# Kernel tuning notes

Hardware: AMD Instinct MI355X
Metric: run time of the kernel (lower is better)

The kernel has to match this reference:

```python
import jax, jax.numpy as jnp
import numpy as np

N_NODES = 50000
N_EDGES = 1600000
IN_DIM = 128
HIDDEN = 16
HEADS = 8
OUT_DIM = 64


def setup_inputs() -> dict:
    key = jax.random.key(0)
    k1, k2, k3, k4, k5 = jax.random.split(key, 5)
    h = jax.random.normal(k1, (N_NODES, IN_DIM), dtype=jnp.float32)
    W1 = jax.random.normal(k2, (IN_DIM, HEADS * HIDDEN), dtype=jnp.float32) * (IN_DIM ** -0.5)
    W2 = jax.random.normal(k3, (HEADS * HIDDEN, OUT_DIM), dtype=jnp.float32) * ((HEADS * HIDDEN) ** -0.5)
    src = jax.random.randint(k4, (N_EDGES,), 0, N_NODES, dtype=jnp.int32)
    dst = jax.random.randint(k5, (N_EDGES,), 0, N_NODES, dtype=jnp.int32)
    return {"h": h, "W1": W1, "W2": W2, "src": src, "dst": dst}


def dot_gat_conv(h, W, src, dst, num_heads, out_feats):
    # Project and split heads: [N, H, D]
    feat = (h @ W).reshape(-1, num_heads, out_feats)
    fs = feat[src]                       # [E, H, D] gather
    fd = feat[dst]                       # [E, H, D] gather
    scale = jnp.asarray(out_feats, feat.dtype) ** -0.5
    e = jnp.einsum('ehd,ehd->eh', fs, fd) * scale  # [E, H] scaled dot score
    # Edge softmax over incoming edges of each destination node
    m = jax.ops.segment_max(e, dst, num_segments=N_NODES)   # [N, H]
    m = jnp.where(jnp.isfinite(m), m, jnp.zeros_like(m))    # isolated nodes
    ex = jnp.exp(e - m[dst])                                 # [E, H]
    denom = jax.ops.segment_sum(ex, dst, num_segments=N_NODES)  # [N, H]
    a = ex / jnp.maximum(denom[dst], jnp.asarray(1e-9, ex.dtype))  # [E, H]
    # Weighted scatter-sum aggregation: [N, H, D]
    return jax.ops.segment_sum(a[:, :, None] * fs, dst, num_segments=N_NODES)


def reference(h, W1, W2, src, dst):
    h1 = dot_gat_conv(h, W1, src, dst, HEADS, HIDDEN)  # [N, H, hidden]
    h1 = jax.nn.elu(h1).reshape(N_NODES, HEADS * HIDDEN)  # flatten(1)
    # Dropout: eval-mode identity
    h2 = dot_gat_conv(h1, W2, src, dst, 1, OUT_DIM)  # [N, 1, out]
    return h2.mean(axis=1)  # [N, out]
```

## Files before the change

### kernel.cpp

```cpp
#include <hip/hip_runtime.h>
#include <hip/hip_bf16.h>

#define N_NODES 50000
#define N_EDGES 1600000
#define NBUCK 98
#define EPB 4096
#define NB_A ((N_EDGES + EPB - 1) / EPB)

typedef short bf16x8 __attribute__((ext_vector_type(8)));
typedef float f32x4  __attribute__((ext_vector_type(4)));
typedef float f32x2  __attribute__((ext_vector_type(2)));

__device__ __forceinline__ float bf16_raw_to_f32(unsigned short u) {
    return __uint_as_float(((unsigned)u) << 16);
}
__device__ __forceinline__ unsigned short f32_to_bf16_raw(float v) {
    unsigned u = __float_as_uint(v);
    return (unsigned short)((u + 0x7fffu + ((u >> 16) & 1u)) >> 16);
}
__device__ __forceinline__ float load_elem(const void* p, size_t i, int f) {
    if (f) return ((const float*)p)[i];
    return bf16_raw_to_f32(((const unsigned short*)p)[i]);
}
__device__ __forceinline__ void unpack8v(uint4 u, f32x2* f) {
    f[0] = (f32x2){__uint_as_float(u.x << 16), __uint_as_float(u.x & 0xffff0000u)};
    f[1] = (f32x2){__uint_as_float(u.y << 16), __uint_as_float(u.y & 0xffff0000u)};
    f[2] = (f32x2){__uint_as_float(u.z << 16), __uint_as_float(u.z & 0xffff0000u)};
    f[3] = (f32x2){__uint_as_float(u.w << 16), __uint_as_float(u.w & 0xffff0000u)};
}

__global__ void detect_dtype_kernel(const unsigned short* __restrict__ w1raw,
                                    int* __restrict__ flag, int* __restrict__ bcnt) {
    __shared__ float red[256];
    if (threadIdx.x < NBUCK) bcnt[threadIdx.x] = 0;
    float mx = 0.f;
    for (int i = threadIdx.x * 2; i < 16384; i += 512) {
        float v = fabsf(bf16_raw_to_f32(w1raw[i]));
        if (!isnan(v)) mx = fmaxf(mx, v);
    }
    red[threadIdx.x] = mx;
    __syncthreads();
    for (int s = 128; s > 0; s >>= 1) {
        if (threadIdx.x < s) red[threadIdx.x] = fmaxf(red[threadIdx.x], red[threadIdx.x + s]);
        __syncthreads();
    }
    if (threadIdx.x == 0) flag[0] = (red[0] > 1e4f) ? 1 : 0;
}

#define WPAD 136
__global__ void prep_kernel(const void* __restrict__ W1, const void* __restrict__ W2,
                            unsigned short* __restrict__ W1T,
                            unsigned short* __restrict__ W2T,
                            const int* __restrict__ flag) {
    const int f = *flag;
    int bid = blockIdx.x, tid = threadIdx.x;
    if (bid < 8) {
        int n = bid * 16 + (tid & 15);
        int kb = (tid >> 4) * 8;
        for (int j = 0; j < 8; ++j)
            W1T[n * WPAD + kb + j] = f32_to_bf16_raw(load_elem(W1, (size_t)(kb + j) * 128 + n, f));
    } else {
        int n = (bid - 8) * 16 + (tid & 15);
        int kb = (tid >> 4) * 8;
        for (int j = 0; j < 8; ++j)
            W2T[n * WPAD + kb + j] = f32_to_bf16_raw(load_elem(W2, (size_t)(kb + j) * 64 + n, f));
    }
}

__global__ void bucket_count_kernel(const int* __restrict__ dst,
                                    int* __restrict__ bcnt, int E) {
    __shared__ int hist[NBUCK];
    int t = threadIdx.x;
    if (t < NBUCK) hist[t] = 0;
    __syncthreads();
    int e0 = blockIdx.x * EPB;
    for (int k = 0; k < 16; ++k) {
        int e = e0 + k * 256 + t;
        if (e < E) atomicAdd(&hist[dst[e] >> 9], 1);
    }
    __syncthreads();
    if (t < NBUCK && hist[t]) atomicAdd(&bcnt[t], hist[t]);
}

__global__ void bucket_scan_kernel(const int* __restrict__ bcnt,
                                   int* __restrict__ bbase, int* __restrict__ bcur) {
    __shared__ int tmp[128];
    int t = threadIdx.x;
    int v = (t < NBUCK) ? bcnt[t] : 0;
    tmp[t] = v;
    __syncthreads();
    for (int off = 1; off < 128; off <<= 1) {
        int x = (t >= off) ? tmp[t - off] : 0;
        __syncthreads();
        tmp[t] += x;
        __syncthreads();
    }
    if (t < NBUCK) { int ex = tmp[t] - v; bbase[t] = ex; bcur[t] = ex; }
    if (t == NBUCK - 1) bbase[NBUCK] = tmp[t];
}

__global__ void binA_kernel(const int* __restrict__ src, const int* __restrict__ dst,
                            int* __restrict__ bcur, unsigned* __restrict__ inter, int E) {
    __shared__ int hist[NBUCK], gbase[NBUCK], cur[NBUCK];
    int t = threadIdx.x;
    if (t < NBUCK) hist[t] = 0;
    __syncthreads();
    int e0 = blockIdx.x * EPB;
    for (int k = 0; k < 16; ++k) {
        int e = e0 + k * 256 + t;
        if (e < E) atomicAdd(&hist[dst[e] >> 9], 1);
    }
    __syncthreads();
    if (t < NBUCK) {
        int hv = hist[t];
        gbase[t] = hv ? atomicAdd(&bcur[t], hv) : 0;
        cur[t] = 0;
    }
    __syncthreads();
    for (int k = 0; k < 16; ++k) {
        int e = e0 + k * 256 + t;
        if (e < E) {
            int d = dst[e];
            int b = d >> 9;
            int off = atomicAdd(&cur[b], 1);
            inter[gbase[b] + off] = (unsigned)src[e] | ((unsigned)(d & 511) << 16);
        }
    }
}

__global__ void binB_kernel(const unsigned* __restrict__ inter,
                            const int* __restrict__ bbase,
                            int* __restrict__ csr_src, int* __restrict__ start,
                            int N, int E) {
    int b = blockIdx.x;
    int node0 = b << 9;
    int lo = bbase[b], hi = bbase[b + 1];
    __shared__ int hist[512];
    __shared__ int t2[256];
    int t = threadIdx.x;
    hist[t] = 0; hist[t + 256] = 0;
    __syncthreads();
    for (int e = lo + t; e < hi; e += 256) atomicAdd(&hist[inter[e] >> 16], 1);
    __syncthreads();
    int s0 = hist[2 * t], s1 = hist[2 * t + 1];
    t2[t] = s0 + s1;
    __syncthreads();
    for (int off = 1; off < 256; off <<= 1) {
        int x = (t >= off) ? t2[t - off] : 0;
        __syncthreads();
        t2[t] += x;
        __syncthreads();
    }
    int base = (t == 0) ? 0 : t2[t - 1];
    hist[2 * t] = base;
    hist[2 * t + 1] = base + s0;
    __syncthreads();
    int nodeCnt = min(512, N - node0);
    for (int i = t; i < nodeCnt; i += 256) start[node0 + i] = lo + hist[i];
    if (b == NBUCK - 1 && t == 0) start[N] = E;
    __syncthreads();
    for (int e = lo + t; e < hi; e += 256) {
        unsigned u = inter[e];
        int slot = lo + atomicAdd(&hist[u >> 16], 1);
        csr_src[slot] = (int)(u & 0xffffu);
    }
}

__global__ void gemm1_mfma_kernel(const void* __restrict__ h,
                                  const unsigned short* __restrict__ W1T,
                                  unsigned short* __restrict__ feat1, int N,
                                  const int* __restrict__ flag) {
    const int f = *flag;
    int lane = threadIdx.x & 63;
    int rbase = blockIdx.x * 64 + (threadIdx.x >> 6) * 16;
    int arow = rbase + (lane & 15);
    int arowc = min(arow, N - 1);
    int kb0 = (lane >> 4) * 8;

    f32x4 acc[8];
#pragma unroll
    for (int t = 0; t < 8; ++t) acc[t] = (f32x4){0.f, 0.f, 0.f, 0.f};

#pragma unroll
    for (int ks = 0; ks < 4; ++ks) {
        int kb = ks * 32 + kb0;
        bf16x8 afrag;
        if (f == 0) {
            afrag = *(const bf16x8*)((const unsigned short*)h + (size_t)arowc * 128 + kb);
        } else {
            const float* hp = (const float*)h + (size_t)arowc * 128 + kb;
#pragma unroll
            for (int j = 0; j < 8; ++j) afrag[j] = (short)f32_to_bf16_raw(hp[j]);
        }
#pragma unroll
        for (int t = 0; t < 8; ++t) {
            int n = t * 16 + (lane & 15);
            bf16x8 bfrag = *(const bf16x8*)(W1T + n * WPAD + kb);
            acc[t] = __builtin_amdgcn_mfma_f32_16x16x32_bf16(afrag, bfrag, acc[t], 0, 0, 0);
        }
    }
    int orow0 = rbase + (lane >> 4) * 4;
    int col = lane & 15;
#pragma unroll
    for (int t = 0; t < 8; ++t)
#pragma unroll
        for (int r = 0; r < 4; ++r) {
            int row = orow0 + r;
            if (row < N)
                feat1[(size_t)row * 128 + t * 16 + col] = f32_to_bf16_raw(acc[t][r]);
        }
}

__global__ void gemm2_mfma_kernel(const unsigned short* __restrict__ agg1e,
                                  const unsigned short* __restrict__ W2T,
                                  unsigned short* __restrict__ feat2, int N) {
    int lane = threadIdx.x & 63;
    int rbase = blockIdx.x * 64 + (threadIdx.x >> 6) * 16;
    int arow = rbase + (lane & 15);
    int arowc = min(arow, N - 1);
    int kb0 = (lane >> 4) * 8;

    f32x4 acc[4];
#pragma unroll
    for (int t = 0; t < 4; ++t) acc[t] = (f32x4){0.f, 0.f, 0.f, 0.f};

#pragma unroll
    for (int ks = 0; ks < 4; ++ks) {
        int kb = ks * 32 + kb0;
        bf16x8 afrag = *(const bf16x8*)(agg1e + (size_t)arowc * 128 + kb);
#pragma unroll
        for (int t = 0; t < 4; ++t) {
            int n = t * 16 + (lane & 15);
            bf16x8 bfrag = *(const bf16x8*)(W2T + n * WPAD + kb);
            acc[t] = __builtin_amdgcn_mfma_f32_16x16x32_bf16(afrag, bfrag, acc[t], 0, 0, 0);
        }
    }
    int orow0 = rbase + (lane >> 4) * 4;
    int col = lane & 15;
#pragma unroll
    for (int t = 0; t < 4; ++t)
#pragma unroll
        for (int r = 0; r < 4; ++r) {
            int row = orow0 + r;
            if (row < N)
                feat2[(size_t)row * 64 + t * 16 + col] = f32_to_bf16_raw(acc[t][r]);
        }
}

__global__ void gat1_kernel(const unsigned short* __restrict__ feat1,
                            const int* __restrict__ csr_src,
                            const int* __restrict__ start,
                            unsigned short* __restrict__ agg1e, int N) {
    int wave = blockIdx.x * 4 + (threadIdx.x >> 6);
    if (wave >= N) return;
    int lane = threadIdx.x & 63;
    int grp = lane >> 4, gl = lane & 15;
    const char* fb = (const char*)feat1;
    unsigned loff = (unsigned)gl << 4;
    f32x2 fd2[4];
    unpack8v(*(const uint4*)(fb + (((unsigned)wave << 8) + loff)), fd2);

    float l = 0.f;
    f32x2 acc2[4];
#pragma unroll
    for (int k = 0; k < 4; ++k) acc2[k] = (f32x2){0.f, 0.f};

    int e0 = start[wave], e1 = start[wave + 1];
    int base = e0;
    for (; base + 8 <= e1; base += 8) {
        int s0 = csr_src[base + grp];
        int s1 = csr_src[base + 4 + grp];
        uint4 u0 = *(const uint4*)(fb + (((unsigned)s0 << 8) + loff));
        uint4 u1 = *(const uint4*)(fb + (((unsigned)s1 << 8) + loff));
        f32x2 f02[4], f12[4];
        unpack8v(u0, f02); unpack8v(u1, f12);
        f32x2 p02 = fd2[0] * f02[0];
        f32x2 p12 = fd2[0] * f12[0];
#pragma unroll
        for (int k = 1; k < 4; ++k) { p02 += fd2[k] * f02[k]; p12 += fd2[k] * f12[k]; }
        float p0 = p02.x + p02.y;
        float p1 = p12.x + p12.y;
        p0 += __shfl_xor(p0, 1);
        p1 += __shfl_xor(p1, 1);
        float w0 = __expf(p0 * 0.25f);
        float w1 = __expf(p1 * 0.25f);
        f32x2 w02 = (f32x2){w0, w0}, w12 = (f32x2){w1, w1};
#pragma unroll
        for (int k = 0; k < 4; ++k) {
            acc2[k] += w02 * f02[k];
            acc2[k] += w12 * f12[k];
        }
        l += w0 + w1;
    }
    for (; base < e1; base += 4) {
        int ed = base + grp;
        bool act = ed < e1;
        int s = act ? csr_src[ed] : 0;
        uint4 u = *(const uint4*)(fb + (((unsigned)s << 8) + loff));
        f32x2 fv2[4]; unpack8v(u, fv2);
        f32x2 p2 = fd2[0] * fv2[0];
#pragma unroll
        for (int k = 1; k < 4; ++k) p2 += fd2[k] * fv2[k];
        float p = p2.x + p2.y;
        p += __shfl_xor(p, 1);
        float w = act ? __expf(p * 0.25f) : 0.f;
        f32x2 wv = (f32x2){w, w};
#pragma unroll
        for (int k = 0; k < 4; ++k) acc2[k] += wv * fv2[k];
        l += w;
    }
#pragma unroll
    for (int off = 16; off <= 32; off <<= 1) {
        l += __shfl_xor(l, off);
#pragma unroll
        for (int k = 0; k < 4; ++k) {
            acc2[k].x += __shfl_xor(acc2[k].x, off);
            acc2[k].y += __shfl_xor(acc2[k].y, off);
        }
    }
    if (grp == 0) {
        float rcp = 1.f / fmaxf(l, 1e-9f);
        float v[8];
#pragma unroll
        for (int k = 0; k < 4; ++k) {
            float x0 = acc2[k].x * rcp;
            float x1 = acc2[k].y * rcp;
            v[2 * k]     = (x0 > 0.f) ? x0 : expm1f(x0);
            v[2 * k + 1] = (x1 > 0.f) ? x1 : expm1f(x1);
        }
        uint4 pk;
        pk.x = (unsigned)f32_to_bf16_raw(v[0]) | ((unsigned)f32_to_bf16_raw(v[1]) << 16);
        pk.y = (unsigned)f32_to_bf16_raw(v[2]) | ((unsigned)f32_to_bf16_raw(v[3]) << 16);
        pk.z = (unsigned)f32_to_bf16_raw(v[4]) | ((unsigned)f32_to_bf16_raw(v[5]) << 16);
        pk.w = (unsigned)f32_to_bf16_raw(v[6]) | ((unsigned)f32_to_bf16_raw(v[7]) << 16);
        *(uint4*)(agg1e + (size_t)wave * 128 + gl * 8) = pk;
    }
}

__global__ void gat2_kernel(const unsigned short* __restrict__ feat2,
                            const int* __restrict__ csr_src,
                            const int* __restrict__ start,
                            void* __restrict__ out, int N,
                            const int* __restrict__ flag) {
    int wave = blockIdx.x * 4 + (threadIdx.x >> 6);
    if (wave >= N) return;
    int lane = threadIdx.x & 63;
    int grp = lane >> 3, gl = lane & 7;
    const int f = *flag;
    const char* fb = (const char*)feat2;
    unsigned loff = (unsigned)gl << 4;
    f32x2 fd2[4];
    unpack8v(*(const uint4*)(fb + (((unsigned)wave << 7) + loff)), fd2);

    float l = 0.f;
    f32x2 acc2[4];
#pragma unroll
    for (int k = 0; k < 4; ++k) acc2[k] = (f32x2){0.f, 0.f};

    int e0 = start[wave], e1 = start[wave + 1];
    int base = e0;
    for (; base + 16 <= e1; base += 16) {
        int s0 = csr_src[base + grp];
        int s1 = csr_src[base + 8 + grp];
        uint4 u0 = *(const uint4*)(fb + (((unsigned)s0 << 7) + loff));
        uint4 u1 = *(const uint4*)(fb + (((unsigned)s1 << 7) + loff));
        f32x2 f02[4], f12[4];
        unpack8v(u0, f02); unpack8v(u1, f12);
        f32x2 p02 = fd2[0] * f02[0];
        f32x2 p12 = fd2[0] * f12[0];
#pragma unroll
        for (int k = 1; k < 4; ++k) { p02 += fd2[k] * f02[k]; p12 += fd2[k] * f12[k]; }
        float p0 = p02.x + p02.y;
        float p1 = p12.x + p12.y;
        p0 += __shfl_xor(p0, 1); p1 += __shfl_xor(p1, 1);
        p0 += __shfl_xor(p0, 2); p1 += __shfl_xor(p1, 2);
        p0 += __shfl_xor(p0, 4); p1 += __shfl_xor(p1, 4);
        float w0 = __expf(p0 * 0.125f);
        float w1 = __expf(p1 * 0.125f);
        f32x2 w02 = (f32x2){w0, w0}, w12 = (f32x2){w1, w1};
#pragma unroll
        for (int k = 0; k < 4; ++k) {
            acc2[k] += w02 * f02[k];
            acc2[k] += w12 * f12[k];
        }
        l += w0 + w1;
    }
    for (; base < e1; base += 8) {
        int ed = base + grp;
        bool act = ed < e1;
        int s = act ? csr_src[ed] : 0;
        uint4 u = *(const uint4*)(fb + (((unsigned)s << 7) + loff));
        f32x2 fv2[4]; unpack8v(u, fv2);
        f32x2 p2 = fd2[0] * fv2[0];
#pragma unroll
        for (int k = 1; k < 4; ++k) p2 += fd2[k] * fv2[k];
        float p = p2.x + p2.y;
        p += __shfl_xor(p, 1);
        p += __shfl_xor(p, 2);
        p += __shfl_xor(p, 4);
        float w = act ? __expf(p * 0.125f) : 0.f;
        f32x2 wv = (f32x2){w, w};
#pragma unroll
        for (int k = 0; k < 4; ++k) acc2[k] += wv * fv2[k];
        l += w;
    }
#pragma unroll
    for (int off = 8; off <= 32; off <<= 1) {
        l += __shfl_xor(l, off);
#pragma unroll
        for (int k = 0; k < 4; ++k) {
            acc2[k].x += __shfl_xor(acc2[k].x, off);
            acc2[k].y += __shfl_xor(acc2[k].y, off);
        }
    }
    if (grp == 0) {
        float rcp = 1.f / fmaxf(l, 1e-9f);
        float v[8];
#pragma unroll
        for (int k = 0; k < 4; ++k) {
            v[2 * k]     = acc2[k].x * rcp;
            v[2 * k + 1] = acc2[k].y * rcp;
        }
        if (f) {
            float* op = (float*)out + (size_t)wave * 64 + gl * 8;
            *(float4*)(op)     = (float4){v[0], v[1], v[2], v[3]};
            *(float4*)(op + 4) = (float4){v[4], v[5], v[6], v[7]};
        } else {
            uint4 pk;
            pk.x = (unsigned)f32_to_bf16_raw(v[0]) | ((unsigned)f32_to_bf16_raw(v[1]) << 16);
            pk.y = (unsigned)f32_to_bf16_raw(v[2]) | ((unsigned)f32_to_bf16_raw(v[3]) << 16);
            pk.z = (unsigned)f32_to_bf16_raw(v[4]) | ((unsigned)f32_to_bf16_raw(v[5]) << 16);
            pk.w = (unsigned)f32_to_bf16_raw(v[6]) | ((unsigned)f32_to_bf16_raw(v[7]) << 16);
            *(uint4*)((unsigned short*)out + (size_t)wave * 64 + gl * 8) = pk;
        }
    }
}

extern "C" void kernel_launch(void* const* d_in, const int* in_sizes, int n_in,
                              void* d_out, int out_size, void* d_ws, size_t ws_size,
                              hipStream_t stream) {
    const void* h  = d_in[0];
    const void* W1 = d_in[1];
    const void* W2 = d_in[2];
    const int* src = (const int*)d_in[3];
    const int* dst = (const int*)d_in[4];

    float* ws = (float*)d_ws;
    unsigned short* feat1 = (unsigned short*)ws;
    unsigned short* agg1e = (unsigned short*)(ws + 3200000);
    unsigned short* feat2 = (unsigned short*)ws;
    unsigned* inter       = (unsigned*)(ws + 6400000);
    int*   csr_src        = (int*)(ws + 9600000);
    int*   start          = (int*)(ws + 11200000);
    int*   flag           = (int*)(ws + 11330000);
    int*   bcnt           = (int*)(ws + 11331000);
    int*   bbase          = (int*)(ws + 11332000);
    int*   bcur           = (int*)(ws + 11333000);
    unsigned short* W1T   = (unsigned short*)(ws + 11340000);
    unsigned short* W2T   = (unsigned short*)(ws + 11350000);

    detect_dtype_kernel<<<1, 256, 0, stream>>>((const unsigned short*)W1, flag, bcnt);
    prep_kernel<<<12, 256, 0, stream>>>(W1, W2, W1T, W2T, flag);

    bucket_count_kernel<<<NB_A, 256, 0, stream>>>(dst, bcnt, N_EDGES);
    bucket_scan_kernel<<<1, 128, 0, stream>>>(bcnt, bbase, bcur);
    binA_kernel<<<NB_A, 256, 0, stream>>>(src, dst, bcur, inter, N_EDGES);
    binB_kernel<<<NBUCK, 256, 0, stream>>>(inter, bbase, csr_src, start, N_NODES, N_EDGES);

    gemm1_mfma_kernel<<<(N_NODES + 63) / 64, 256, 0, stream>>>(h, W1T, feat1, N_NODES, flag);
    gat1_kernel<<<(N_NODES + 3) / 4, 256, 0, stream>>>(feat1, csr_src, start, agg1e, N_NODES);
    gemm2_mfma_kernel<<<(N_NODES + 63) / 64, 256, 0, stream>>>(agg1e, W2T, feat2, N_NODES);
    gat2_kernel<<<(N_NODES + 3) / 4, 256, 0, stream>>>(feat2, csr_src, start, d_out, N_NODES, flag);
}
```

Baseline: 283.5 us.

## Sort nodes by degree and process eight destination nodes per wave

Adds a degree histogram in binB, a scan, and a scatter that builds a worklist of nodes sorted by in-degree, highest first. The gat kernels now assign 8 destination nodes per wave, 8 lanes per node, so lanes in a wave have similar edge counts. Each lane covers 16 features in gat1 and 8 in gat2, which removes most cross-group shuffle reductions and the masked tail iterations. The cost is two extra small launches, atomics on the degree counters, and output writes to scattered node rows. Each node's edge list is now walked serially by its 8 lanes, two edges at a time.

```diff
diff --git a/kernel.cpp b/kernel.cpp
--- a/kernel.cpp
+++ b/kernel.cpp
@@ -6,6 +6,7 @@
 #define NBUCK 98
 #define EPB 4096
 #define NB_A ((N_EDGES + EPB - 1) / EPB)
+#define DEGBINS 512
 
 typedef short bf16x8 __attribute__((ext_vector_type(8)));
 typedef float f32x4  __attribute__((ext_vector_type(4)));
@@ -30,9 +31,12 @@
 }
 
 __global__ void detect_dtype_kernel(const unsigned short* __restrict__ w1raw,
-                                    int* __restrict__ flag, int* __restrict__ bcnt) {
+                                    int* __restrict__ flag, int* __restrict__ bcnt,
+                                    int* __restrict__ ghist) {
     __shared__ float red[256];
     if (threadIdx.x < NBUCK) bcnt[threadIdx.x] = 0;
+    ghist[threadIdx.x] = 0;
+    ghist[threadIdx.x + 256] = 0;
     float mx = 0.f;
     for (int i = threadIdx.x * 2; i < 16384; i += 512) {
         float v = fabsf(bf16_raw_to_f32(w1raw[i]));
@@ -131,6 +135,7 @@
 __global__ void binB_kernel(const unsigned* __restrict__ inter,
                             const int* __restrict__ bbase,
                             int* __restrict__ csr_src, int* __restrict__ start,
+                            int* __restrict__ ghist,
                             int N, int E) {
     int b = blockIdx.x;
     int node0 = b << 9;
@@ -143,6 +148,9 @@
     for (int e = lo + t; e < hi; e += 256) atomicAdd(&hist[inter[e] >> 16], 1);
     __syncthreads();
     int s0 = hist[2 * t], s1 = hist[2 * t + 1];
+    int nodeCnt = min(512, N - node0);
+    if (2 * t < nodeCnt)     atomicAdd(&ghist[min(s0, DEGBINS - 1)], 1);
+    if (2 * t + 1 < nodeCnt) atomicAdd(&ghist[min(s1, DEGBINS - 1)], 1);
     t2[t] = s0 + s1;
     __syncthreads();
     for (int off = 1; off < 256; off <<= 1) {
@@ -155,7 +163,6 @@
     hist[2 * t] = base;
     hist[2 * t + 1] = base + s0;
     __syncthreads();
-    int nodeCnt = min(512, N - node0);
     for (int i = t; i < nodeCnt; i += 256) start[node0 + i] = lo + hist[i];
     if (b == NBUCK - 1 && t == 0) start[N] = E;
     __syncthreads();
@@ -164,6 +171,31 @@
         int slot = lo + atomicAdd(&hist[u >> 16], 1);
         csr_src[slot] = (int)(u & 0xffffu);
     }
+}
+
+__global__ void degscan_kernel(const int* __restrict__ ghist, int* __restrict__ gcur) {
+    __shared__ int tmp[DEGBINS];
+    int t = threadIdx.x;
+    int v = ghist[t];
+    tmp[t] = v;
+    __syncthreads();
+    for (int off = 1; off < DEGBINS; off <<= 1) {
+        int x = (t >= off) ? tmp[t - off] : 0;
+        __syncthreads();
+        tmp[t] += x;
+        __syncthreads();
+    }
+    gcur[t] = tmp[t] - v;
+}
+
+__global__ void degscatter_kernel(const int* __restrict__ start,
+                                  int* __restrict__ gcur,
+                                  int* __restrict__ wl, int N) {
+    int i = blockIdx.x * 256 + threadIdx.x;
+    if (i >= N) return;
+    int deg = start[i + 1] - start[i];
+    int off = atomicAdd(&gcur[min(deg, DEGBINS - 1)], 1);
+    wl[N - 1 - off] = i;
 }
 
 __global__ void gemm1_mfma_kernel(const void* __restrict__ h,
@@ -250,189 +282,170 @@
 __global__ void gat1_kernel(const unsigned short* __restrict__ feat1,
                             const int* __restrict__ csr_src,
                             const int* __restrict__ start,
+                            const int* __restrict__ wl,
                             unsigned short* __restrict__ agg1e, int N) {
     int wave = blockIdx.x * 4 + (threadIdx.x >> 6);
-    if (wave >= N) return;
     int lane = threadIdx.x & 63;
-    int grp = lane >> 4, gl = lane & 15;
+    int g = lane >> 3, gl = lane & 7;
+    int nidx = wave * 8 + g;
+    if (nidx >= N) return;
+    int dstn = wl[nidx];
+
     const char* fb = (const char*)feat1;
+    unsigned loff = (unsigned)gl << 5;
+    unsigned drow = ((unsigned)dstn << 8) + loff;
+    f32x2 fd2[8];
+    unpack8v(*(const uint4*)(fb + drow), fd2);
+    unpack8v(*(const uint4*)(fb + drow + 16), fd2 + 4);
+
+    float l = 0.f;
+    f32x2 acc2[8];
+#pragma unroll
+    for (int k = 0; k < 8; ++k) acc2[k] = (f32x2){0.f, 0.f};
+
+    int e0 = start[dstn], e1 = start[dstn + 1];
+    int base = e0;
+    for (; base + 2 <= e1; base += 2) {
+        int s0 = csr_src[base], s1 = csr_src[base + 1];
+        const char* r0 = fb + ((unsigned)s0 << 8) + loff;
+        const char* r1 = fb + ((unsigned)s1 << 8) + loff;
+        uint4 a0 = *(const uint4*)r0, a1 = *(const uint4*)(r0 + 16);
+        uint4 b0 = *(const uint4*)r1, b1 = *(const uint4*)(r1 + 16);
+        f32x2 f0[8], f1[8];
+        unpack8v(a0, f0); unpack8v(a1, f0 + 4);
+        unpack8v(b0, f1); unpack8v(b1, f1 + 4);
+        f32x2 p0 = fd2[0] * f0[0];
+        f32x2 p1 = fd2[0] * f1[0];
+#pragma unroll
+        for (int k = 1; k < 8; ++k) { p0 += fd2[k] * f0[k]; p1 += fd2[k] * f1[k]; }
+        float q0 = p0.x + p0.y;
+        float q1 = p1.x + p1.y;
+        float w0 = __expf(q0 * 0.25f);
+        float w1 = __expf(q1 * 0.25f);
+        f32x2 W0 = (f32x2){w0, w0}, W1 = (f32x2){w1, w1};
+#pragma unroll
+        for (int k = 0; k < 8; ++k) {
+            acc2[k] += W0 * f0[k];
+            acc2[k] += W1 * f1[k];
+        }
+        l += w0 + w1;
+    }
+    if (base < e1) {
+        int s = csr_src[base];
+        const char* r0 = fb + ((unsigned)s << 8) + loff;
+        uint4 a0 = *(const uint4*)r0, a1 = *(const uint4*)(r0 + 16);
+        f32x2 fv[8];
+        unpack8v(a0, fv); unpack8v(a1, fv + 4);
+        f32x2 p = fd2[0] * fv[0];
+#pragma unroll
+        for (int k = 1; k < 8; ++k) p += fd2[k] * fv[k];
+        float w = __expf((p.x + p.y) * 0.25f);
+        f32x2 W = (f32x2){w, w};
+#pragma unroll
+        for (int k = 0; k < 8; ++k) acc2[k] += W * fv[k];
+        l += w;
+    }
+    float rcp = 1.f / fmaxf(l, 1e-9f);
+    unsigned pk[8];
+#pragma unroll
+    for (int k = 0; k < 8; ++k) {
+        float x0 = acc2[k].x * rcp, x1 = acc2[k].y * rcp;
+        x0 = (x0 > 0.f) ? x0 : expm1f(x0);
+        x1 = (x1 > 0.f) ? x1 : expm1f(x1);
+        pk[k] = (unsigned)f32_to_bf16_raw(x0) | ((unsigned)f32_to_bf16_raw(x1) << 16);
+    }
+    *(uint4*)((char*)agg1e + drow)      = (uint4){pk[0], pk[1], pk[2], pk[3]};
+    *(uint4*)((char*)agg1e + drow + 16) = (uint4){pk[4], pk[5], pk[6], pk[7]};
+}
+
+__global__ void gat2_kernel(const unsigned short* __restrict__ feat2,
+                            const int* __restrict__ csr_src,
+                            const int* __restrict__ start,
+                            const int* __restrict__ wl,
+                            void* __restrict__ out, int N,
+                            const int* __restrict__ flag) {
+    int wave = blockIdx.x * 4 + (threadIdx.x >> 6);
+    int lane = threadIdx.x & 63;
+    int g = lane >> 3, gl = lane & 7;
+    int nidx = wave * 8 + g;
+    if (nidx >= N) return;
+    int dstn = wl[nidx];
+    const int f = *flag;
+
+    const char* fb = (const char*)feat2;
     unsigned loff = (unsigned)gl << 4;
+    unsigned drow = ((unsigned)dstn << 7) + loff;
     f32x2 fd2[4];
-    unpack8v(*(const uint4*)(fb + (((unsigned)wave << 8) + loff)), fd2);
+    unpack8v(*(const uint4*)(fb + drow), fd2);
 
     float l = 0.f;
     f32x2 acc2[4];
 #pragma unroll
     for (int k = 0; k < 4; ++k) acc2[k] = (f32x2){0.f, 0.f};
 
-    int e0 = start[wave], e1 = start[wave + 1];
+    int e0 = start[dstn], e1 = start[dstn + 1];
     int base = e0;
-    for (; base + 8 <= e1; base += 8) {
-        int s0 = csr_src[base + grp];
-        int s1 = csr_src[base + 4 + grp];
-        uint4 u0 = *(const uint4*)(fb + (((unsigned)s0 << 8) + loff));
-        uint4 u1 = *(const uint4*)(fb + (((unsigned)s1 << 8) + loff));
-        f32x2 f02[4], f12[4];
-        unpack8v(u0, f02); unpack8v(u1, f12);
-        f32x2 p02 = fd2[0] * f02[0];
-        f32x2 p12 = fd2[0] * f12[0];
-#pragma unroll
-        for (int k = 1; k < 4; ++k) { p02 += fd2[k] * f02[k]; p12 += fd2[k] * f12[k]; }
-        float p0 = p02.x + p02.y;
-        float p1 = p12.x + p12.y;
-        p0 += __shfl_xor(p0, 1);
-        p1 += __shfl_xor(p1, 1);
-        float w0 = __expf(p0 * 0.25f);
-        float w1 = __expf(p1 * 0.25f);
-        f32x2 w02 = (f32x2){w0, w0}, w12 = (f32x2){w1, w1};
+    for (; base + 2 <= e1; base += 2) {
+        int s0 = csr_src[base], s1 = csr_src[base + 1];
+        uint4 u0 = *(const uint4*)(fb + ((unsigned)s0 << 7) + loff);
+        uint4 u1 = *(const uint4*)(fb + ((unsigned)s1 << 7) + loff);
+        f32x2 f0[4], f1[4];
+        unpack8v(u0, f0); unpack8v(u1, f1);
+        f32x2 p0 = fd2[0] * f0[0];
+        f32x2 p1 = fd2[0] * f1[0];
+#pragma unroll
+        for (int k = 1; k < 4; ++k) { p0 += fd2[k] * f0[k]; p1 += fd2[k] * f1[k]; }
+        float q0 = p0.x + p0.y;
+        float q1 = p1.x + p1.y;
+        q0 += __shfl_xor(q0, 1); q1 += __shfl_xor(q1, 1);
+        q0 += __shfl_xor(q0, 2); q1 += __shfl_xor(q1, 2);
+        q0 += __shfl_xor(q0, 4); q1 += __shfl_xor(q1, 4);
+        float w0 = __expf(q0 * 0.125f);
+        float w1 = __expf(q1 * 0.125f);
+        f32x2 W0 = (f32x2){w0, w0}, W1 = (f32x2){w1, w1};
 #pragma unroll
         for (int k = 0; k < 4; ++k) {
-            acc2[k] += w02 * f02[k];
-            acc2[k] += w12 * f12[k];
+            acc2[k] += W0 * f0[k];
+            acc2[k] += W1 * f1[k];
         }
         l += w0 + w1;
     }
-    for (; base < e1; base += 4) {
-        int ed = base + grp;
-        bool act = ed < e1;
-        int s = act ? csr_src[ed] : 0;
-        uint4 u = *(const uint4*)(fb + (((unsigned)s << 8) + loff));
-        f32x2 fv2[4]; unpack8v(u, fv2);
-        f32x2 p2 = fd2[0] * fv2[0];
-#pragma unroll
-        for (int k = 1; k < 4; ++k) p2 += fd2[k] * fv2[k];
-        float p = p2.x + p2.y;
-        p += __shfl_xor(p, 1);
-        float w = act ? __expf(p * 0.25f) : 0.f;
-        f32x2 wv = (f32x2){w, w};
-#pragma unroll
-        for (int k = 0; k < 4; ++k) acc2[k] += wv * fv2[k];
+    if (base < e1) {
+        int s = csr_src[base];
+        uint4 u = *(const uint4*)(fb + ((unsigned)s << 7) + loff);
+        f32x2 fv[4];
+        unpack8v(u, fv);
+        f32x2 p = fd2[0] * fv[0];
+#pragma unroll
+        for (int k = 1; k < 4; ++k) p += fd2[k] * fv[k];
+        float q = p.x + p.y;
+        q += __shfl_xor(q, 1);
+        q += __shfl_xor(q, 2);
+        q += __shfl_xor(q, 4);
+        float w = __expf(q * 0.125f);
+        f32x2 W = (f32x2){w, w};
+#pragma unroll
+        for (int k = 0; k < 4; ++k) acc2[k] += W * fv[k];
         l += w;
     }
-#pragma unroll
-    for (int off = 16; off <= 32; off <<= 1) {
-        l += __shfl_xor(l, off);
-#pragma unroll
-        for (int k = 0; k < 4; ++k) {
-            acc2[k].x += __shfl_xor(acc2[k].x, off);
-            acc2[k].y += __shfl_xor(acc2[k].y, off);
-        }
-    }
-    if (grp == 0) {
-        float rcp = 1.f / fmaxf(l, 1e-9f);
-        float v[8];
-#pragma unroll
-        for (int k = 0; k < 4; ++k) {
-            float x0 = acc2[k].x * rcp;
-            float x1 = acc2[k].y * rcp;
-            v[2 * k]     = (x0 > 0.f) ? x0 : expm1f(x0);
-            v[2 * k + 1] = (x1 > 0.f) ? x1 : expm1f(x1);
-        }
+    float rcp = 1.f / fmaxf(l, 1e-9f);
+    float v[8];
+#pragma unroll
+    for (int k = 0; k < 4; ++k) {
+        v[2 * k]     = acc2[k].x * rcp;
+        v[2 * k + 1] = acc2[k].y * rcp;
+    }
+    if (f) {
+        float* op = (float*)out + ((size_t)dstn << 6) + (gl << 3);
+        *(float4*)(op)     = (float4){v[0], v[1], v[2], v[3]};
+        *(float4*)(op + 4) = (float4){v[4], v[5], v[6], v[7]};
+    } else {
         uint4 pk;
         pk.x = (unsigned)f32_to_bf16_raw(v[0]) | ((unsigned)f32_to_bf16_raw(v[1]) << 16);
         pk.y = (unsigned)f32_to_bf16_raw(v[2]) | ((unsigned)f32_to_bf16_raw(v[3]) << 16);
         pk.z = (unsigned)f32_to_bf16_raw(v[4]) | ((unsigned)f32_to_bf16_raw(v[5]) << 16);
         pk.w = (unsigned)f32_to_bf16_raw(v[6]) | ((unsigned)f32_to_bf16_raw(v[7]) << 16);
-        *(uint4*)(agg1e + (size_t)wave * 128 + gl * 8) = pk;
-    }
-}
-
-__global__ void gat2_kernel(const unsigned short* __restrict__ feat2,
-                            const int* __restrict__ csr_src,
-                            const int* __restrict__ start,
-                            void* __restrict__ out, int N,
-                            const int* __restrict__ flag) {
-    int wave = blockIdx.x * 4 + (threadIdx.x >> 6);
-    if (wave >= N) return;
-    int lane = threadIdx.x & 63;
-    int grp = lane >> 3, gl = lane & 7;
-    const int f = *flag;
-    const char* fb = (const char*)feat2;
-    unsigned loff = (unsigned)gl << 4;
-    f32x2 fd2[4];
-    unpack8v(*(const uint4*)(fb + (((unsigned)wave << 7) + loff)), fd2);
-
-    float l = 0.f;
-    f32x2 acc2[4];
-#pragma unroll
-    for (int k = 0; k < 4; ++k) acc2[k] = (f32x2){0.f, 0.f};
-
-    int e0 = start[wave], e1 = start[wave + 1];
-    int base = e0;
-    for (; base + 16 <= e1; base += 16) {
-        int s0 = csr_src[base + grp];
-        int s1 = csr_src[base + 8 + grp];
-        uint4 u0 = *(const uint4*)(fb + (((unsigned)s0 << 7) + loff));
-        uint4 u1 = *(const uint4*)(fb + (((unsigned)s1 << 7) + loff));
-        f32x2 f02[4], f12[4];
-        unpack8v(u0, f02); unpack8v(u1, f12);
-        f32x2 p02 = fd2[0] * f02[0];
-        f32x2 p12 = fd2[0] * f12[0];
-#pragma unroll
-        for (int k = 1; k < 4; ++k) { p02 += fd2[k] * f02[k]; p12 += fd2[k] * f12[k]; }
-        float p0 = p02.x + p02.y;
-        float p1 = p12.x + p12.y;
-        p0 += __shfl_xor(p0, 1); p1 += __shfl_xor(p1, 1);
-        p0 += __shfl_xor(p0, 2); p1 += __shfl_xor(p1, 2);
-        p0 += __shfl_xor(p0, 4); p1 += __shfl_xor(p1, 4);
-        float w0 = __expf(p0 * 0.125f);
-        float w1 = __expf(p1 * 0.125f);
-        f32x2 w02 = (f32x2){w0, w0}, w12 = (f32x2){w1, w1};
-#pragma unroll
-        for (int k = 0; k < 4; ++k) {
-            acc2[k] += w02 * f02[k];
-            acc2[k] += w12 * f12[k];
-        }
-        l += w0 + w1;
-    }
-    for (; base < e1; base += 8) {
-        int ed = base + grp;
-        bool act = ed < e1;
-        int s = act ? csr_src[ed] : 0;
-        uint4 u = *(const uint4*)(fb + (((unsigned)s << 7) + loff));
-        f32x2 fv2[4]; unpack8v(u, fv2);
-        f32x2 p2 = fd2[0] * fv2[0];
-#pragma unroll
-        for (int k = 1; k < 4; ++k) p2 += fd2[k] * fv2[k];
-        float p = p2.x + p2.y;
-        p += __shfl_xor(p, 1);
-        p += __shfl_xor(p, 2);
-        p += __shfl_xor(p, 4);
-        float w = act ? __expf(p * 0.125f) : 0.f;
-        f32x2 wv = (f32x2){w, w};
-#pragma unroll
-        for (int k = 0; k < 4; ++k) acc2[k] += wv * fv2[k];
-        l += w;
-    }
-#pragma unroll
-    for (int off = 8; off <= 32; off <<= 1) {
-        l += __shfl_xor(l, off);
-#pragma unroll
-        for (int k = 0; k < 4; ++k) {
-            acc2[k].x += __shfl_xor(acc2[k].x, off);
-            acc2[k].y += __shfl_xor(acc2[k].y, off);
-        }
-    }
-    if (grp == 0) {
-        float rcp = 1.f / fmaxf(l, 1e-9f);
-        float v[8];
-#pragma unroll
-        for (int k = 0; k < 4; ++k) {
-            v[2 * k]     = acc2[k].x * rcp;
-            v[2 * k + 1] = acc2[k].y * rcp;
-        }
-        if (f) {
-            float* op = (float*)out + (size_t)wave * 64 + gl * 8;
-            *(float4*)(op)     = (float4){v[0], v[1], v[2], v[3]};
-            *(float4*)(op + 4) = (float4){v[4], v[5], v[6], v[7]};
-        } else {
-            uint4 pk;
-            pk.x = (unsigned)f32_to_bf16_raw(v[0]) | ((unsigned)f32_to_bf16_raw(v[1]) << 16);
-            pk.y = (unsigned)f32_to_bf16_raw(v[2]) | ((unsigned)f32_to_bf16_raw(v[3]) << 16);
-            pk.z = (unsigned)f32_to_bf16_raw(v[4]) | ((unsigned)f32_to_bf16_raw(v[5]) << 16);
-            pk.w = (unsigned)f32_to_bf16_raw(v[6]) | ((unsigned)f32_to_bf16_raw(v[7]) << 16);
-            *(uint4*)((unsigned short*)out + (size_t)wave * 64 + gl * 8) = pk;
-        }
+        *(uint4*)((unsigned short*)out + ((size_t)dstn << 6) + (gl << 3)) = pk;
     }
 }
 
@@ -450,25 +463,32 @@
     unsigned short* agg1e = (unsigned short*)(ws + 3200000);
     unsigned short* feat2 = (unsigned short*)ws;
     unsigned* inter       = (unsigned*)(ws + 6400000);
+    int*   wl             = (int*)(ws + 6400000);
     int*   csr_src        = (int*)(ws + 9600000);
     int*   start          = (int*)(ws + 11200000);
     int*   flag           = (int*)(ws + 11330000);
     int*   bcnt           = (int*)(ws + 11331000);
     int*   bbase          = (int*)(ws + 11332000);
     int*   bcur           = (int*)(ws + 11333000);
+    int*   ghist          = (int*)(ws + 11334000);
+    int*   gcur           = (int*)(ws + 11335000);
     unsigned short* W1T   = (unsigned short*)(ws + 11340000);
     unsigned short* W2T   = (unsigned short*)(ws + 11350000);
 
-    detect_dtype_kernel<<<1, 256, 0, stream>>>((const unsigned short*)W1, flag, bcnt);
+    detect_dtype_kernel<<<1, 256, 0, stream>>>((const unsigned short*)W1, flag, bcnt, ghist);
     prep_kernel<<<12, 256, 0, stream>>>(W1, W2, W1T, W2T, flag);
 
     bucket_count_kernel<<<NB_A, 256, 0, stream>>>(dst, bcnt, N_EDGES);
     bucket_scan_kernel<<<1, 128, 0, stream>>>(bcnt, bbase, bcur);
     binA_kernel<<<NB_A, 256, 0, stream>>>(src, dst, bcur, inter, N_EDGES);
-    binB_kernel<<<NBUCK, 256, 0, stream>>>(inter, bbase, csr_src, start, N_NODES, N_EDGES);
+    binB_kernel<<<NBUCK, 256, 0, stream>>>(inter, bbase, csr_src, start, ghist, N_NODES, N_EDGES);
+
+    degscan_kernel<<<1, DEGBINS, 0, stream>>>(ghist, gcur);
+    degscatter_kernel<<<(N_NODES + 255) / 256, 256, 0, stream>>>(start, gcur, wl, N_NODES);
 
     gemm1_mfma_kernel<<<(N_NODES + 63) / 64, 256, 0, stream>>>(h, W1T, feat1, N_NODES, flag);
-    gat1_kernel<<<(N_NODES + 3) / 4, 256, 0, stream>>>(feat1, csr_src, start, agg1e, N_NODES);
+    int nwaves = (N_NODES + 7) / 8;
+    gat1_kernel<<<(nwaves + 3) / 4, 256, 0, stream>>>(feat1, csr_src, start, wl, agg1e, N_NODES);
     gemm2_mfma_kernel<<<(N_NODES + 63) / 64, 256, 0, stream>>>(agg1e, W2T, feat2, N_NODES);
-    gat2_kernel<<<(N_NODES + 3) / 4, 256, 0, stream>>>(feat2, csr_src, start, d_out, N_NODES, flag);
-}
+    gat2_kernel<<<(nwaves + 3) / 4, 256, 0, stream>>>(feat2, csr_src, start, wl, d_out, N_NODES, flag);
+}
```

After: 520.3 us. 1.84x slower.
